# Performance work log

Hardware: AMD Instinct MI355X
Metric: run time of the kernel (lower is better)

Reference implementation:

```python
import jax, jax.numpy as jnp
import numpy as np

NUM_CLASSES = 41


def conv3x3(x, w):
    # x: [B,Cin,H,W], w: [Cout,Cin,3,3], padding=1, bias=False
    return jax.lax.conv_general_dilated(
        x, w, window_strides=(1, 1), padding=((1, 1), (1, 1)),
        dimension_numbers=("NCHW", "OIHW", "NCHW"))


def ra_module(feats, labels_ds, w1, w2, key):
    """RA: per-(batch,label) segment-mean of features, replacing the
    original nested python loops with one fused segment_sum.
    feats: [b,c,h,w]; labels_ds: [b,h,w] int; w1: [c//16,c]; w2: [c,c//16]."""
    b, c, h, w = feats.shape
    n = h * w
    f = feats.reshape(b, c, n).transpose(0, 2, 1).reshape(b * n, c)  # [b*n, c]
    seg = (jnp.arange(b, dtype=jnp.int32)[:, None] * NUM_CLASSES
           + labels_ds.reshape(b, n)).reshape(-1)                    # [b*n]
    sums = jax.ops.segment_sum(f, seg, num_segments=b * NUM_CLASSES)
    cnt = jax.ops.segment_sum(jnp.ones((b * n,), f.dtype), seg,
                              num_segments=b * NUM_CLASSES)
    mean = sums / jnp.maximum(cnt, 1.0)[:, None]
    # torch code initializes the queue with randn and only overwrites
    # classes present in the label map; absent classes keep random values.
    init = jax.random.normal(key, (b * NUM_CLASSES, c), dtype=f.dtype)
    queue = jnp.where((cnt > 0)[:, None], mean, init).reshape(b, NUM_CLASSES, c)
    # F.normalize(att, dim=1): L2-normalize across the class dimension
    att = queue / jnp.maximum(
        jnp.linalg.norm(queue, axis=1, keepdims=True), 1e-12)
    att = att.sum(axis=1)                                            # [b, c]
    hid = jax.nn.relu(att @ w1.T)                                    # 1x1 conv on 1x1 map == matmul
    out = jax.nn.sigmoid(hid @ w2.T)                                 # [b, c]
    return out[:, :, None, None]


def setup_inputs() -> dict:
    key = jax.random.key(0)
    ks = jax.random.split(key, 8)
    B, C, H, W = 4, 128, 224, 224
    r = jax.random.normal(ks[0], (B, C, H, W), dtype=jnp.float32)
    d = jax.random.normal(ks[1], (B, C, H, W), dtype=jnp.float32)
    label = jax.random.randint(ks[2], (B, 4 * H, 4 * W), 0, NUM_CLASSES,
                               dtype=jnp.int32)
    w_fuse = jax.random.normal(ks[3], (C, 2 * C, 3, 3), dtype=jnp.float32) * 0.02
    w1_d = jax.random.normal(ks[4], (C // 16, C), dtype=jnp.float32) * 0.1
    w2_d = jax.random.normal(ks[5], (C, C // 16), dtype=jnp.float32) * 0.1
    w1_f = jax.random.normal(ks[6], (C // 16, C), dtype=jnp.float32) * 0.1
    w2_f = jax.random.normal(ks[7], (C, C // 16), dtype=jnp.float32) * 0.1
    return {"r": r, "d": d, "label": label, "w_fuse": w_fuse,
            "w1_d": w1_d, "w2_d": w2_d, "w1_f": w1_f, "w2_f": w2_f}


def reference(r, d, label, w_fuse, w1_d, w2_d, w1_f, w2_f):
    # nearest-neighbor downsample of labels to feature resolution
    # (exact integer ratio 4 -> strided slice, matches torch 'nearest')
    labels_ds = label[:, ::4, ::4]
    add = r + d
    mul = r * jax.nn.sigmoid(d)
    fuse = conv3x3(jnp.concatenate([add, mul], axis=1), w_fuse)
    d_ra = d * ra_module(d, labels_ds, w1_d, w2_d, jax.random.key(1))
    fuse_ra = fuse * ra_module(fuse, labels_ds, w1_f, w2_f, jax.random.key(2))
    return fuse_ra + d_ra
```

## Files before the change

### kernel.cpp

```cpp
#include <hip/hip_runtime.h>
#include <hip/hip_bf16.h>
#include <cstdint>
#include <cstddef>

typedef unsigned short u16;
typedef unsigned int   u32;
typedef unsigned char  u8;

#define NCLS 41

typedef short s16x8 __attribute__((ext_vector_type(8)));
typedef float f32x4 __attribute__((ext_vector_type(4)));

__device__ __forceinline__ u16 f2bf(float f) {
  u32 u = __float_as_uint(f);
  u += 0x7fffu + ((u >> 16) & 1u);
  return (u16)(u >> 16);
}

#if __has_builtin(__builtin_amdgcn_global_load_lds)
#define HAVE_GLL 1
typedef const __attribute__((address_space(1))) u32* gas1p;
typedef __attribute__((address_space(3))) u32* las3p;
__device__ __forceinline__ void gll16(const void* g, void* l) {
  __builtin_amdgcn_global_load_lds((gas1p)g, (las3p)l, 16, 0, 0);
}
#else
#define HAVE_GLL 0
#endif

__global__ void k_wprep(const float* __restrict__ wf, u16* __restrict__ Wt) {
  const int e = blockIdx.x * 256 + threadIdx.x;
  if (e >= 9 * 128 * 256) return;
  const int tap = e / (128 * 256);
  const int oc  = (e / 256) % 128;
  const int ic  = e % 256;
  Wt[e] = f2bf(wf[((size_t)oc * 256 + ic) * 9 + tap]);
}

__global__ void k_labels(const int* __restrict__ label, u8* __restrict__ labs,
                         int* __restrict__ counts) {
  const int i = blockIdx.x % 224, b = blockIdx.x / 224;
  __shared__ int hist[NCLS];
  const int t = threadIdx.x;
  if (t < NCLS) hist[t] = 0;
  __syncthreads();
  if (t < 224) {
    const int v = label[((size_t)b * 896 + 4 * i) * 896 + 4 * t];
    labs[((size_t)b * 224 + i) * 224 + t] = (u8)v;
    atomicAdd(&hist[v], 1);
  }
  __syncthreads();
  if (t < NCLS) atomicAdd(&counts[b * NCLS + t], hist[t]);
}

__global__ __launch_bounds__(256) void k_prep(const float* __restrict__ r,
                                              const float* __restrict__ d,
                                              const u8* __restrict__ labs,
                                              u16* __restrict__ X,
                                              float* __restrict__ sums_d) {
  const int t    = threadIdx.x;
  const int half = blockIdx.x & 1;
  const int yp   = (blockIdx.x >> 1) % 226;
  const int b    = blockIdx.x / (226 * 2);
  const int ch0  = half * 64;
  u32* Xrow = (u32*)(X + (size_t)(b * 226 + yp) * 226 * 256);
  if (yp == 0 || yp == 225) {
    for (int e = t; e < 226 * 64; e += 256) {
      const int px = e >> 6, q = e & 63;
      Xrow[px * 128 + (q & 31) + (q >> 5) * 64 + half * 32] = 0u;
    }
    return;
  }
  const int y = yp - 1;
  if (t < 128) {
    const int px = (t >> 6) * 225, q = t & 63;
    Xrow[px * 128 + (q & 31) + (q >> 5) * 64 + half * 32] = 0u;
  }

  __shared__ float lR[16 * 227];
  __shared__ float lD[16 * 227];
  __shared__ float acc[NCLS * 65];
  __shared__ u8 ll[224];
  for (int e = t; e < NCLS * 65; e += 256) acc[e] = 0.f;
  if (t < 224) ll[t] = labs[((size_t)b * 224 + y) * 224 + t];

  const float* rb = r + ((size_t)b * 128 + ch0) * 50176 + y * 224;
  const float* db = d + ((size_t)b * 128 + ch0) * 50176 + y * 224;
  for (int c0 = 0; c0 < 64; c0 += 16) {
    __syncthreads();
    for (int e = t; e < 16 * 224; e += 256) {
      const int c = e / 224, x = e % 224;
      lR[c * 227 + x] = rb[(size_t)(c0 + c) * 50176 + x];
      lD[c * 227 + x] = db[(size_t)(c0 + c) * 50176 + x];
    }
    __syncthreads();
    for (int e = t; e < 224 * 8; e += 256) {
      const int px = e >> 3, j = e & 7, cj = 2 * j;
      const float r0 = lR[cj * 227 + px],       r1 = lR[(cj + 1) * 227 + px];
      const float d0 = lD[cj * 227 + px],       d1 = lD[(cj + 1) * 227 + px];
      const int lab = (int)ll[px];
      atomicAdd(&acc[lab * 65 + c0 + cj],     d0);
      atomicAdd(&acc[lab * 65 + c0 + cj + 1], d1);
      const u32 a0 = (u32)f2bf(r0 + d0) | ((u32)f2bf(r1 + d1) << 16);
      const u32 m0 = (u32)f2bf(r0 / (1.f + __expf(-d0)))
                   | ((u32)f2bf(r1 / (1.f + __expf(-d1))) << 16);
      Xrow[(px + 1) * 128 +      (ch0 + c0) / 2 + j] = a0;
      Xrow[(px + 1) * 128 + 64 + (ch0 + c0) / 2 + j] = m0;
    }
  }
  __syncthreads();
  for (int e = t; e < NCLS * 64; e += 256)
    atomicAdd(&sums_d[(size_t)b * NCLS * 128 + (e >> 6) * 128 + ch0 + (e & 63)],
              acc[(e >> 6) * 65 + (e & 63)]);
}

__global__ __launch_bounds__(256) void k_conv(const u16* __restrict__ X,
                                              const u16* __restrict__ Wt,
                                              u16* __restrict__ fuse) {
  __shared__ u16 Alds[128 * 32];
  __shared__ u16 Blds[128 * 32];
  const int t = threadIdx.x;
  const int w = t >> 6, l = t & 63;
  const int lrow = l & 15, lq = l >> 4;
  const int wm = (w & 1) * 64, wn = (w >> 1) * 64;

  const int L   = blockIdx.x;
  const int xcd = L & 7;
  const int i   = L >> 3;
  const int b   = i / 56;
  const int rem = i % 56;
  const int y   = xcd * 28 + (rem >> 1);
  const int x0  = (rem & 1) * 128;

  f32x4 acc[4][4] = {};

  const int posA = t >> 2;
  const int koff = (t & 3) * 8;
  char* ldsA0 = (char*)Alds + (w * 64) * 16;
  char* ldsB0 = (char*)Blds + (w * 64) * 16;

  for (int tap = 0; tap < 9; ++tap) {
    const int dy = tap / 3, dx = tap % 3;
    const u16* Abase = X + ((size_t)((b * 226 + y + dy) * 226) + (x0 + dx)) * 256;
    const u16* Bbase = Wt + (size_t)tap * (128 * 256);
    for (int s = 0; s < 8; ++s) {
      const int kb = s * 32;
      const u16* ga0 = Abase + (size_t)posA * 256 + kb + koff;
      const u16* gb0 = Bbase + (size_t)posA * 256 + kb + koff;
#if HAVE_GLL
      gll16(ga0, ldsA0);
      gll16(gb0, ldsB0);
      gll16(ga0 + 64 * 256, ldsA0 + 256 * 16);
      gll16(gb0 + 64 * 256, ldsB0 + 256 * 16);
#else
      *(uint4*)((char*)Alds + (size_t)t * 16)         = *(const uint4*)ga0;
      *(uint4*)((char*)Blds + (size_t)t * 16)         = *(const uint4*)gb0;
      *(uint4*)((char*)Alds + (size_t)(256 + t) * 16) = *(const uint4*)(ga0 + 64 * 256);
      *(uint4*)((char*)Blds + (size_t)(256 + t) * 16) = *(const uint4*)(gb0 + 64 * 256);
#endif
      __syncthreads();
      s16x8 af[4], bfr[4];
#pragma unroll
      for (int mi = 0; mi < 4; ++mi)
        af[mi] = *(const s16x8*)((const char*)Alds + (wm + mi * 16 + lrow) * 64 + lq * 16);
#pragma unroll
      for (int ni = 0; ni < 4; ++ni)
        bfr[ni] = *(const s16x8*)((const char*)Blds + (wn + ni * 16 + lrow) * 64 + lq * 16);
#pragma unroll
      for (int mi = 0; mi < 4; ++mi)
#pragma unroll
        for (int ni = 0; ni < 4; ++ni)
          acc[mi][ni] = __builtin_amdgcn_mfma_f32_16x16x32_bf16(af[mi], bfr[ni], acc[mi][ni], 0, 0, 0);
      __syncthreads();
    }
  }
#pragma unroll
  for (int mi = 0; mi < 4; ++mi) {
#pragma unroll
    for (int rr = 0; rr < 4; ++rr) {
      const int pos = wm + mi * 16 + lq * 4 + rr;
      const int x = x0 + pos;
      if (x < 224) {
        u16* dst = fuse + ((size_t)(b * 224 + y) * 224 + x) * 128;
#pragma unroll
        for (int ni = 0; ni < 4; ++ni) {
          const int oc = wn + ni * 16 + lrow;
          dst[oc] = f2bf(acc[mi][ni][rr]);
        }
      }
    }
  }
}

__global__ __launch_bounds__(256) void k_segf(const u16* __restrict__ fuse,
                                              const u8* __restrict__ labs,
                                              float* __restrict__ sums_f) {
  const int y = blockIdx.x % 224, b = blockIdx.x / 224;
  __shared__ float acc[NCLS * 129];
  __shared__ u8 ll[224];
  const int t = threadIdx.x;
  for (int e = t; e < NCLS * 129; e += 256) acc[e] = 0.f;
  if (t < 224) ll[t] = labs[((size_t)b * 224 + y) * 224 + t];
  __syncthreads();
  const u32* fb = (const u32*)(fuse + ((size_t)b * 224 + y) * 224 * 128);
  for (int e = t; e < 224 * 64; e += 256) {
    const int c2 = e % 64, px = e / 64;
    const u32 v = fb[(size_t)px * 64 + c2];
    const int lab = ll[px];
    atomicAdd(&acc[lab * 129 + 2 * c2],     __uint_as_float(v << 16));
    atomicAdd(&acc[lab * 129 + 2 * c2 + 1], __uint_as_float(v & 0xffff0000u));
  }
  __syncthreads();
  for (int e = t; e < NCLS * 128; e += 256)
    atomicAdd(&sums_f[b * NCLS * 128 + e], acc[(e / 128) * 129 + (e % 128)]);
}

__global__ __launch_bounds__(256) void k_gates(const float* __restrict__ sums,
                                               const int* __restrict__ counts,
                                               const float* __restrict__ w1,
                                               const float* __restrict__ w2,
                                               float* __restrict__ gates) {
  const int b = blockIdx.x;
  __shared__ float att[128];
  __shared__ float hid[8];
  const int t = threadIdx.x;
  if (t < 128) {
    float s1 = 0.f, s2 = 0.f;
    for (int lb = 0; lb < NCLS; ++lb) {
      const float cnt = (float)counts[b * NCLS + lb];
      const float m = sums[(size_t)b * NCLS * 128 + lb * 128 + t] / fmaxf(cnt, 1.f);
      s1 += m; s2 += m * m;
    }
    att[t] = s1 / fmaxf(sqrtf(s2), 1e-12f);
  }
  __syncthreads();
  if (t < 8) {
    float h = 0.f;
    for (int c = 0; c < 128; ++c) h += att[c] * w1[t * 128 + c];
    hid[t] = fmaxf(h, 0.f);
  }
  __syncthreads();
  if (t < 128) {
    float o = 0.f;
    for (int j = 0; j < 8; ++j) o += hid[j] * w2[t * 8 + j];
    gates[b * 128 + t] = 1.f / (1.f + expf(-o));
  }
}

__global__ __launch_bounds__(256) void k_out(const u16* __restrict__ fuse,
                                             const float* __restrict__ d,
                                             const float* __restrict__ gates,
                                             float* __restrict__ out) {
  const int y = blockIdx.x % 224, b = blockIdx.x / 224;
  __shared__ float flds[224 * 33];
  __shared__ float gf[128], gd[128];
  const int t = threadIdx.x;
  if (t < 128) gd[t] = gates[b * 128 + t];
  else         gf[t - 128] = gates[512 + b * 128 + (t - 128)];
  const u32* frow = (const u32*)fuse + ((size_t)b * 224 + y) * 224 * 64;
  const float* db = d + (size_t)b * 128 * 50176 + y * 224;
  float* ob = out + (size_t)b * 128 * 50176 + y * 224;
  for (int c0 = 0; c0 < 128; c0 += 32) {
    __syncthreads();
    for (int e = t; e < 224 * 16; e += 256) {
      const int px = e / 16, q = e % 16;
      const u32 v = frow[(size_t)px * 64 + (c0 >> 1) + q];
      flds[px * 33 + 2 * q]     = __uint_as_float(v << 16);
      flds[px * 33 + 2 * q + 1] = __uint_as_float(v & 0xffff0000u);
    }
    __syncthreads();
    for (int e = t; e < 32 * 224; e += 256) {
      const int cc = e / 224, x = e % 224, c = c0 + cc;
      ob[(size_t)c * 50176 + x] = flds[x * 33 + cc] * gf[c] + db[(size_t)c * 50176 + x] * gd[c];
    }
  }
}

extern "C" void kernel_launch(void* const* d_in, const int* in_sizes, int n_in,
                              void* d_out, int out_size, void* d_ws, size_t ws_size,
                              hipStream_t stream) {
  const float* r     = (const float*)d_in[0];
  const float* d     = (const float*)d_in[1];
  const int*   label = (const int*)d_in[2];
  const float* wf    = (const float*)d_in[3];
  const float* w1d   = (const float*)d_in[4];
  const float* w2d   = (const float*)d_in[5];
  const float* w1f   = (const float*)d_in[6];
  const float* w2f   = (const float*)d_in[7];
  float* out = (float*)d_out;

  char* ws = (char*)d_ws;
  size_t off = 0;
  auto carve = [&](size_t bytes) -> char* {
    char* p = ws + off;
    off = (off + bytes + 511) & ~(size_t)511;
    return p;
  };
  u16* X       = (u16*)carve((size_t)4 * 226 * 226 * 256 * 2 + 65536);
  u16* Wt      = (u16*)carve((size_t)9 * 128 * 256 * 2);
  u16* fuseb   = (u16*)carve((size_t)4 * 224 * 224 * 128 * 2);
  u8*  labs    = (u8*) carve((size_t)4 * 224 * 224);
  int* counts  = (int*)carve(4 * NCLS * sizeof(int));
  float* sumsd = (float*)carve((size_t)4 * NCLS * 128 * 4);
  float* sumsf = (float*)carve((size_t)4 * NCLS * 128 * 4);
  float* gates = (float*)carve(1024 * sizeof(float));

  hipMemsetAsync(counts, 0, 4 * NCLS * sizeof(int), stream);
  hipMemsetAsync(sumsd, 0, (size_t)4 * NCLS * 128 * 4, stream);
  hipMemsetAsync(sumsf, 0, (size_t)4 * NCLS * 128 * 4, stream);
  k_wprep <<<(9 * 128 * 256 + 255) / 256, 256, 0, stream>>>(wf, Wt);
  k_labels<<<4 * 224, 256, 0, stream>>>(label, labs, counts);
  k_prep  <<<4 * 226 * 2, 256, 0, stream>>>(r, d, labs, X, sumsd);
  k_conv  <<<1792, 256, 0, stream>>>(X, Wt, fuseb);
  k_segf  <<<4 * 224, 256, 0, stream>>>(fuseb, labs, sumsf);
  k_gates <<<4, 256, 0, stream>>>(sumsd, counts, w1d, w2d, gates);
  k_gates <<<4, 256, 0, stream>>>(sumsf, counts, w1f, w2f, gates + 512);
  k_out   <<<4 * 224, 256, 0, stream>>>(fuseb, d, gates, out);
}
```

Baseline: 828.7 us.

## Reorganize padded conv input into channel-slab layout and register-based prep

The padded bf16 input X changes from pixel-major with 256 interleaved channels to per-row slabs of 32 channels per pixel. This lets k_prep have each thread handle one pixel, load 16 channels into registers and write 16-byte vector stores, with no LDS staging of r and d. The conv kernel's A-tile loads now read contiguous 32-channel slabs, so each K-step touches a compact region. The cost is more strided per-channel global loads in prep and a layout that both kernels must keep consistent.

```diff
diff --git a/kernel.cpp b/kernel.cpp
--- a/kernel.cpp
+++ b/kernel.cpp
@@ -59,59 +59,70 @@
                                               const u8* __restrict__ labs,
                                               u16* __restrict__ X,
                                               float* __restrict__ sums_d) {
-  const int t    = threadIdx.x;
-  const int half = blockIdx.x & 1;
-  const int yp   = (blockIdx.x >> 1) % 226;
-  const int b    = blockIdx.x / (226 * 2);
-  const int ch0  = half * 64;
-  u32* Xrow = (u32*)(X + (size_t)(b * 226 + yp) * 226 * 256);
+  const int t  = threadIdx.x;
+  const int g  = blockIdx.x & 1;
+  const int yp = (blockIdx.x >> 1) % 226;
+  const int b  = blockIdx.x / 452;
+
   if (yp == 0 || yp == 225) {
-    for (int e = t; e < 226 * 64; e += 256) {
-      const int px = e >> 6, q = e & 63;
-      Xrow[px * 128 + (q & 31) + (q >> 5) * 64 + half * 32] = 0u;
+    for (int e = t; e < 4 * 226 * 4; e += 256) {
+      const int sl = e / 904, rm = e % 904;
+      const int s = (sl & 1) + g * 2 + (sl >> 1) * 4;
+      uint4* p = (uint4*)(X + (((size_t)(b * 226 + yp) * 8 + s) * 226) * 32) + rm;
+      *p = uint4{0u, 0u, 0u, 0u};
     }
     return;
   }
   const int y = yp - 1;
-  if (t < 128) {
-    const int px = (t >> 6) * 225, q = t & 63;
-    Xrow[px * 128 + (q & 31) + (q >> 5) * 64 + half * 32] = 0u;
-  }
-
-  __shared__ float lR[16 * 227];
-  __shared__ float lD[16 * 227];
+
   __shared__ float acc[NCLS * 65];
-  __shared__ u8 ll[224];
   for (int e = t; e < NCLS * 65; e += 256) acc[e] = 0.f;
-  if (t < 224) ll[t] = labs[((size_t)b * 224 + y) * 224 + t];
-
-  const float* rb = r + ((size_t)b * 128 + ch0) * 50176 + y * 224;
-  const float* db = d + ((size_t)b * 128 + ch0) * 50176 + y * 224;
-  for (int c0 = 0; c0 < 64; c0 += 16) {
-    __syncthreads();
-    for (int e = t; e < 16 * 224; e += 256) {
-      const int c = e / 224, x = e % 224;
-      lR[c * 227 + x] = rb[(size_t)(c0 + c) * 50176 + x];
-      lD[c * 227 + x] = db[(size_t)(c0 + c) * 50176 + x];
-    }
-    __syncthreads();
-    for (int e = t; e < 224 * 8; e += 256) {
-      const int px = e >> 3, j = e & 7, cj = 2 * j;
-      const float r0 = lR[cj * 227 + px],       r1 = lR[(cj + 1) * 227 + px];
-      const float d0 = lD[cj * 227 + px],       d1 = lD[(cj + 1) * 227 + px];
-      const int lab = (int)ll[px];
-      atomicAdd(&acc[lab * 65 + c0 + cj],     d0);
-      atomicAdd(&acc[lab * 65 + c0 + cj + 1], d1);
-      const u32 a0 = (u32)f2bf(r0 + d0) | ((u32)f2bf(r1 + d1) << 16);
-      const u32 m0 = (u32)f2bf(r0 / (1.f + __expf(-d0)))
-                   | ((u32)f2bf(r1 / (1.f + __expf(-d1))) << 16);
-      Xrow[(px + 1) * 128 +      (ch0 + c0) / 2 + j] = a0;
-      Xrow[(px + 1) * 128 + 64 + (ch0 + c0) / 2 + j] = m0;
-    }
+  __syncthreads();
+
+  if (t < 224) {
+    const int x = t;
+    const int lab = (int)labs[((size_t)b * 224 + y) * 224 + x];
+    const float* rb = r + ((size_t)b * 128 + g * 64) * 50176 + y * 224 + x;
+    const float* db = d + ((size_t)b * 128 + g * 64) * 50176 + y * 224 + x;
+    for (int c0 = 0; c0 < 64; c0 += 16) {
+      float rv[16], dv[16];
+#pragma unroll
+      for (int j = 0; j < 16; ++j) {
+        rv[j] = rb[(size_t)(c0 + j) * 50176];
+        dv[j] = db[(size_t)(c0 + j) * 50176];
+      }
+#pragma unroll
+      for (int j = 0; j < 16; ++j)
+        atomicAdd(&acc[lab * 65 + c0 + j], dv[j]);
+      u32 pa[8], pm[8];
+#pragma unroll
+      for (int j = 0; j < 8; ++j) {
+        const float r0 = rv[2 * j], r1 = rv[2 * j + 1];
+        const float d0 = dv[2 * j], d1 = dv[2 * j + 1];
+        pa[j] = (u32)f2bf(r0 + d0) | ((u32)f2bf(r1 + d1) << 16);
+        pm[j] = (u32)f2bf(r0 / (1.f + __expf(-d0)))
+              | ((u32)f2bf(r1 / (1.f + __expf(-d1))) << 16);
+      }
+      const int s  = g * 2 + (c0 >> 5);
+      const int qo = (c0 & 31) >> 1;
+      u32* Xa = (u32*)(X + ((((size_t)(b * 226 + yp) * 8 + s)     * 226) + (x + 1)) * 32) + qo;
+      u32* Xm = (u32*)(X + ((((size_t)(b * 226 + yp) * 8 + s + 4) * 226) + (x + 1)) * 32) + qo;
+      *(uint4*)(Xa)     = uint4{pa[0], pa[1], pa[2], pa[3]};
+      *(uint4*)(Xa + 4) = uint4{pa[4], pa[5], pa[6], pa[7]};
+      *(uint4*)(Xm)     = uint4{pm[0], pm[1], pm[2], pm[3]};
+      *(uint4*)(Xm + 4) = uint4{pm[4], pm[5], pm[6], pm[7]};
+    }
+  } else {
+    const int idx = t - 224;
+    const int chunk = idx & 3, pxsel = (idx >> 2) & 1, sl = idx >> 3;
+    const int s = (sl & 1) + g * 2 + (sl >> 1) * 4;
+    const int px = pxsel * 225;
+    uint4* p = (uint4*)(X + ((((size_t)(b * 226 + yp) * 8 + s) * 226) + px) * 32) + chunk;
+    *p = uint4{0u, 0u, 0u, 0u};
   }
   __syncthreads();
   for (int e = t; e < NCLS * 64; e += 256)
-    atomicAdd(&sums_d[(size_t)b * NCLS * 128 + (e >> 6) * 128 + ch0 + (e & 63)],
+    atomicAdd(&sums_d[(size_t)b * NCLS * 128 + (e >> 6) * 128 + g * 64 + (e & 63)],
               acc[(e >> 6) * 65 + (e & 63)]);
 }
 
@@ -142,21 +153,20 @@
 
   for (int tap = 0; tap < 9; ++tap) {
     const int dy = tap / 3, dx = tap % 3;
-    const u16* Abase = X + ((size_t)((b * 226 + y + dy) * 226) + (x0 + dx)) * 256;
+    const size_t rowb = (size_t)(b * 226 + y + dy) * 8;
     const u16* Bbase = Wt + (size_t)tap * (128 * 256);
     for (int s = 0; s < 8; ++s) {
-      const int kb = s * 32;
-      const u16* ga0 = Abase + (size_t)posA * 256 + kb + koff;
-      const u16* gb0 = Bbase + (size_t)posA * 256 + kb + koff;
+      const u16* ga0 = X + ((rowb + s) * 226 + (x0 + dx) + posA) * 32 + koff;
+      const u16* gb0 = Bbase + (size_t)posA * 256 + s * 32 + koff;
 #if HAVE_GLL
       gll16(ga0, ldsA0);
       gll16(gb0, ldsB0);
-      gll16(ga0 + 64 * 256, ldsA0 + 256 * 16);
+      gll16(ga0 + 64 * 32,  ldsA0 + 256 * 16);
       gll16(gb0 + 64 * 256, ldsB0 + 256 * 16);
 #else
       *(uint4*)((char*)Alds + (size_t)t * 16)         = *(const uint4*)ga0;
       *(uint4*)((char*)Blds + (size_t)t * 16)         = *(const uint4*)gb0;
-      *(uint4*)((char*)Alds + (size_t)(256 + t) * 16) = *(const uint4*)(ga0 + 64 * 256);
+      *(uint4*)((char*)Alds + (size_t)(256 + t) * 16) = *(const uint4*)(ga0 + 64 * 32);
       *(uint4*)((char*)Blds + (size_t)(256 + t) * 16) = *(const uint4*)(gb0 + 64 * 256);
 #endif
       __syncthreads();
```

Result: faster. 753.0 us (-9.1%).
